# Kernel optimization log

Hardware: AMD Instinct MI355X
Metric: run time of the kernel (lower is better)

Reference implementation:

```python
import jax, jax.numpy as jnp
import numpy as np

N, D, C = 16384, 64, 128
MARGIN = 1.0
EPS_NORM = 1e-6   # F.normalize eps
EPS_PD = 1e-6     # F.pairwise_distance eps (added to the difference elementwise)


def setup_inputs() -> dict:
    key = jax.random.key(0)
    embeddings = jax.random.normal(key, (N, D), dtype=jnp.float32)
    labels = (jnp.arange(N) % C).astype(jnp.int32).reshape(N, 1)
    # deterministic valid positive: same label (i % C), different index
    pos_idx = ((jnp.arange(N) + C) % N).astype(jnp.int32)
    return {"embeddings": embeddings, "labels": labels, "pos_idx": pos_idx}


def reference(embeddings, labels, pos_idx):
    # L2-normalize rows (torch F.normalize: x / max(||x||, eps))
    nrm = jnp.linalg.norm(embeddings, axis=1, keepdims=True)
    e = embeddings / jnp.maximum(nrm, EPS_NORM)

    lab = labels[:, 0]
    # torch pairwise_distance computes ||x1 - x2 + eps||_2, eps added per element:
    # ||xi - xj + eps||^2 = ||xi||^2 + ||xj||^2 - 2 xi.xj + 2*eps*(sum(xi)-sum(xj)) + D*eps^2
    sq = jnp.sum(e * e, axis=1)          # [N]
    s = jnp.sum(e, axis=1)               # [N]
    gram = e @ e.T                        # [N, N]
    d2 = (sq[:, None] + sq[None, :] - 2.0 * gram
          + 2.0 * EPS_PD * (s[:, None] - s[None, :]) + D * EPS_PD * EPS_PD)
    d2 = jnp.maximum(d2, 0.0)
    dist = jnp.sqrt(jnp.maximum(d2, 1e-12))  # guard sqrt grad at 0

    # one positive per anchor: squared distance
    pos_loss = jnp.sum(d2[jnp.arange(N), pos_idx])

    # all negatives per anchor: hinge^2 on (margin - dist)
    neg_mask = lab[:, None] != lab[None, :]
    hinge = jnp.maximum(MARGIN - dist, 0.0)
    neg_loss = jnp.sum(jnp.where(neg_mask, hinge * hinge, 0.0))

    n_comparisons = N + jnp.sum(neg_mask)
    return (pos_loss + neg_loss) / n_comparisons.astype(jnp.float32)
```

## Files before the change

### kernel.cpp

```cpp
#include <hip/hip_runtime.h>
#include <hip/hip_bf16.h>

#define NN 16384
#define DD 64
#define NBI 32
#define NUNITS 2112
#define NBLK 512
#define NPOSB (NN/4)
#define SCREEN_T 0.49f

constexpr float F_EPS_PD   = 1e-6f;
constexpr float F_EPS_NORM = 1e-6f;

using bf16x8 = __attribute__((ext_vector_type(8))) short;
using f32x4  = __attribute__((ext_vector_type(4))) float;
typedef __attribute__((address_space(1))) const unsigned int gu32_t;
typedef __attribute__((address_space(3))) unsigned int       lu32_t;

__device__ __forceinline__ float wave_sum_f(float v) {
    #pragma unroll
    for (int o = 32; o >= 1; o >>= 1) v += __shfl_xor(v, o);
    return v;
}

__device__ __forceinline__ int band_off(int I) { return 2 * I * (65 - I); }

__global__ __launch_bounds__(256) void norm_kernel(
    const float* __restrict__ emb, const int* __restrict__ pidx,
    const int* __restrict__ lab, float2* __restrict__ up,
    float2* __restrict__ vcp, __hip_bfloat16* __restrict__ ebf,
    float* __restrict__ posP) {
    int w    = threadIdx.x >> 6;
    int row  = blockIdx.x * 4 + w;
    int lane = threadIdx.x & 63;
    int j    = pidx[row];
    float x  = emb[(size_t)row * DD + lane];
    float xj = emb[(size_t)j   * DD + lane];

    float n2  = wave_sum_f(x * x);
    float sx  = wave_sum_f(x);
    float n2j = wave_sum_f(xj * xj);
    float sxj = wave_sum_f(xj);
    float dot = wave_sum_f(x * xj);

    float m  = fmaxf(sqrtf(n2),  F_EPS_NORM);
    float mj = fmaxf(sqrtf(n2j), F_EPS_NORM);
    ebf[(size_t)row * DD + lane] = __float2bfloat16(x / m);

    __shared__ float spos[4];
    if (lane == 0) {
        float sq  = n2 / (m * m);
        float sqj = n2j / (mj * mj);
        float s   = sx / m;
        float sj  = sxj / mj;
        float g   = dot / (m * mj);
        float lf  = (float)lab[row];
        up[row]  = make_float2(sq + 2.0f * F_EPS_PD * s, lf);
        vcp[row] = make_float2(
            sq - 2.0f * F_EPS_PD * s + (float)DD * F_EPS_PD * F_EPS_PD, lf);
        float d2p = sq + sqj - 2.0f * g + 2.0f * F_EPS_PD * (s - sj)
                  + (float)DD * F_EPS_PD * F_EPS_PD;
        spos[w] = fmaxf(d2p, 0.0f);
    }
    __syncthreads();
    if (threadIdx.x == 0)
        posP[blockIdx.x] = spos[0] + spos[1] + spos[2] + spos[3];
}

__device__ __forceinline__ void stage_tile(const short* ebf, const float2* vcp,
                                           int tile, short* slotB, float2* slotV,
                                           int w, int lane) {
    const short* tbase = ebf + (size_t)tile * (128 * DD);
    int rlo = lane >> 3;
    int g   = (lane & 7) ^ rlo;
    #pragma unroll
    for (int q = 0; q < 2; ++q) {
        int m = w * 2 + q;
        __builtin_amdgcn_global_load_lds(
            (gu32_t*)(const void*)(tbase + (size_t)(8 * m + rlo) * DD + g * 8),
            (lu32_t*)(void*)(slotB + m * 512), 16, 0, 0);
    }
    __builtin_amdgcn_global_load_lds(
        (gu32_t*)(const void*)(vcp + (size_t)tile * 128 + lane * 2),
        (lu32_t*)(void*)slotV, 16, 0, 0);
}

#define MFMA_STEP(CD, t_)                                                      \
    do {                                                                       \
        const short* rowp_ = lb + ((t_) * 16 + lrow) * 64;                     \
        bf16x8 b0_ = *(const bf16x8*)(rowp_ + c0s);                            \
        bf16x8 b1_ = *(const bf16x8*)(rowp_ + c1s);                            \
        __builtin_amdgcn_s_setprio(1);                                         \
        _Pragma("unroll")                                                      \
        for (int s_ = 0; s_ < 4; ++s_) {                                       \
            f32x4 z_ = {0.f, 0.f, 0.f, 0.f};                                   \
            z_ = __builtin_amdgcn_mfma_f32_16x16x32_bf16(a[s_][0], b0_, z_, 0, 0, 0); \
            z_ = __builtin_amdgcn_mfma_f32_16x16x32_bf16(a[s_][1], b1_, z_, 0, 0, 0); \
            CD[s_] = z_;                                                       \
        }                                                                      \
        __builtin_amdgcn_s_setprio(0);                                         \
    } while (0)

#define SCREEN_STEP(CS, t_)                                                    \
    do {                                                                       \
        float mx_ = fmaxf(fmaxf(CS[0][0], CS[0][1]), fmaxf(CS[0][2], CS[0][3])); \
        mx_ = fmaxf(mx_, fmaxf(fmaxf(CS[1][0], CS[1][1]), fmaxf(CS[1][2], CS[1][3]))); \
        mx_ = fmaxf(mx_, fmaxf(fmaxf(CS[2][0], CS[2][1]), fmaxf(CS[2][2], CS[2][3]))); \
        mx_ = fmaxf(mx_, fmaxf(fmaxf(CS[3][0], CS[3][1]), fmaxf(CS[3][2], CS[3][3]))); \
        if (__any(mx_ > SCREEN_T)) {                                           \
            float2 vl_ = lv[(t_) * 16 + lrow];                                 \
            _Pragma("unroll")                                                  \
            for (int s_ = 0; s_ < 4; ++s_) {                                   \
                _Pragma("unroll")                                              \
                for (int r_ = 0; r_ < 4; ++r_) {                               \
                    float2 ul_ = uband[w * 64 + 16 * s_ + lkh * 4 + r_];       \
                    float d2_ = fmaf(-2.0f, CS[s_][r_], ul_.x + vl_.x);        \
                    float d_  = sqrtf(fmaxf(d2_, 1e-12f));                     \
                    float h_  = fmaxf(1.0f - d_, 0.0f);                        \
                    if (ul_.y != vl_.y) hp = fmaf(h_, h_, hp);                 \
                }                                                              \
            }                                                                  \
        }                                                                      \
    } while (0)

__global__ __launch_bounds__(512, 4) void pair_kernel(
    const short* __restrict__ ebf, const float2* __restrict__ up,
    const float2* __restrict__ vcp, float* __restrict__ negP) {
    __shared__ short  ringB[3][8192];
    __shared__ float2 ringV[3][128];
    __shared__ float2 uband[512];
    __shared__ float  sred[8];
    int tid  = threadIdx.x;
    int w    = tid >> 6;
    int lane = tid & 63;
    int lrow = lane & 15, lkh = lane >> 4;
    int c0s  = ((lkh)     ^ (lrow & 7)) * 8;
    int c1s  = ((lkh + 4) ^ (lrow & 7)) * 8;

    int ks = (int)(((long long)blockIdx.x * NUNITS) / NBLK);
    int ke = (int)(((long long)(blockIdx.x + 1) * NUNITS) / NBLK);

    int I = (int)((65.0f - sqrtf(4225.0f - 2.0f * (float)ks)) * 0.5f);
    I = I < 0 ? 0 : (I > NBI - 1 ? NBI - 1 : I);
    while (band_off(I) > ks) --I;
    while (I < NBI - 1 && band_off(I + 1) <= ks) ++I;

    float hacc = 0.0f;
    int u0 = ks;
    while (u0 < ke) {
        int bend = band_off(I + 1);
        int n    = (ke < bend ? ke : bend) - u0;
        int tj0  = 4 * I + (u0 - band_off(I));
        int rowbase = I * 512 + w * 64;
        int rt      = 4 * I + (w >> 1);

        bf16x8 a[4][2];
        #pragma unroll
        for (int s = 0; s < 4; ++s) {
            const short* ab = ebf + (size_t)(rowbase + 16 * s + lrow) * DD + lkh * 8;
            a[s][0] = *(const bf16x8*)(ab);
            a[s][1] = *(const bf16x8*)(ab + 32);
        }
        if (w < 4)
            __builtin_amdgcn_global_load_lds(
                (gu32_t*)(const void*)(up + (size_t)I * 512 + w * 128 + lane * 2),
                (lu32_t*)(void*)(uband + w * 128), 16, 0, 0);
        stage_tile(ebf, vcp, tj0, &ringB[0][0], &ringV[0][0], w, lane);
        if (n > 1)
            stage_tile(ebf, vcp, tj0 + 1, &ringB[1][0], &ringV[1][0], w, lane);

        int sl = 0;
        for (int k = 0; k < n; ++k) {
            if (k + 1 < n) asm volatile("s_waitcnt vmcnt(3)" ::: "memory");
            else           asm volatile("s_waitcnt vmcnt(0)" ::: "memory");
            __builtin_amdgcn_s_barrier();
            __builtin_amdgcn_sched_barrier(0);
            int sl2 = (sl >= 1) ? sl - 1 : 2;
            if (k + 2 < n)
                stage_tile(ebf, vcp, tj0 + k + 2, &ringB[sl2][0], &ringV[sl2][0],
                           w, lane);

            int tj = tj0 + k;
            float wgt = (tj == rt) ? 1.0f : ((tj > rt) ? 2.0f : 0.0f);
            if (wgt != 0.0f) {
                const short*  lb = &ringB[sl][0];
                const float2* lv = &ringV[sl][0];
                float hp = 0.0f;
                f32x4 cA[4], cB[4];
                MFMA_STEP(cA, 0);
                MFMA_STEP(cB, 1);
                SCREEN_STEP(cA, 0);
                MFMA_STEP(cA, 2);
                SCREEN_STEP(cB, 1);
                MFMA_STEP(cB, 3);
                SCREEN_STEP(cA, 2);
                MFMA_STEP(cA, 4);
                SCREEN_STEP(cB, 3);
                MFMA_STEP(cB, 5);
                SCREEN_STEP(cA, 4);
                MFMA_STEP(cA, 6);
                SCREEN_STEP(cB, 5);
                MFMA_STEP(cB, 7);
                SCREEN_STEP(cA, 6);
                SCREEN_STEP(cB, 7);
                hacc = fmaf(wgt, hp, hacc);
            }
            sl = (sl + 1 == 3) ? 0 : sl + 1;
        }
        __builtin_amdgcn_s_barrier();
        __builtin_amdgcn_sched_barrier(0);
        u0 += n;
        ++I;
    }

    hacc = wave_sum_f(hacc);
    if (lane == 0) sred[w] = hacc;
    __syncthreads();
    if (tid == 0) {
        float tn = 0.f;
        #pragma unroll
        for (int i = 0; i < 8; ++i) tn += sred[i];
        negP[blockIdx.x] = tn;
    }
}

__global__ __launch_bounds__(1024) void reduce_kernel(
    const float* __restrict__ posP, const float* __restrict__ negP,
    const int* __restrict__ lab, float* __restrict__ out) {
    __shared__ unsigned int hist[4][1024];
    int t = threadIdx.x;
    int w = t >> 6, lane = t & 63;
    for (int i = t; i < 4096; i += 1024) hist[i >> 10][i & 1023] = 0u;
    __syncthreads();
    const int4* lab4 = (const int4*)lab;
    for (int i = t; i < NN / 4; i += 1024) {
        int4 v = lab4[i];
        atomicAdd(&hist[w & 3][v.x & 1023], 1u);
        atomicAdd(&hist[w & 3][v.y & 1023], 1u);
        atomicAdd(&hist[w & 3][v.z & 1023], 1u);
        atomicAdd(&hist[w & 3][v.w & 1023], 1u);
    }
    __syncthreads();

    float ps = 0.f, ns = 0.f;
    unsigned long long sqc = 0u;
    const float4* posP4 = (const float4*)posP;
    for (int i = t; i < NPOSB / 4; i += 1024) {
        float4 v = posP4[i];
        ps += (v.x + v.y) + (v.z + v.w);
    }
    if (t < NBLK) ns = negP[t];
    for (int i = t; i < 1024; i += 1024) {
        unsigned long long h = (unsigned long long)hist[0][i] + hist[1][i]
                             + hist[2][i] + hist[3][i];
        sqc += h * h;
    }

    ps = wave_sum_f(ps);
    ns = wave_sum_f(ns);
    #pragma unroll
    for (int o = 32; o >= 1; o >>= 1) sqc += __shfl_xor(sqc, o);

    __shared__ float sp[16], sn[16];
    __shared__ unsigned long long sc[16];
    if (lane == 0) { sp[w] = ps; sn[w] = ns; sc[w] = sqc; }
    __syncthreads();
    if (t == 0) {
        float pos = 0.f, neg = 0.f;
        unsigned long long s2 = 0;
        #pragma unroll
        for (int i = 0; i < 16; ++i) { pos += sp[i]; neg += sn[i]; s2 += sc[i]; }
        unsigned long long nneg = (unsigned long long)NN * NN - s2;
        float ncomp = (float)((unsigned long long)NN + nneg);
        out[0] = (pos + neg) / ncomp;
    }
}

extern "C" void kernel_launch(void* const* d_in, const int* in_sizes, int n_in,
                              void* d_out, int out_size, void* d_ws, size_t ws_size,
                              hipStream_t stream) {
    const float* emb = (const float*)d_in[0];
    const int* lab   = (const int*)d_in[1];
    const int* pidx  = (const int*)d_in[2];
    float* out = (float*)d_out;
    char* ws = (char*)d_ws;
    float2*         up   = (float2*)(ws);
    float2*         vcp  = (float2*)(ws + 131072);
    __hip_bfloat16* ebf  = (__hip_bfloat16*)(ws + 262144);
    float*          posP = (float*)(ws + 2359296);
    float*          negP = (float*)(ws + 2375680);

    norm_kernel<<<NPOSB, 256, 0, stream>>>(emb, pidx, lab, up, vcp, ebf, posP);
    pair_kernel<<<NBLK, 512, 0, stream>>>((const short*)ebf, up, vcp, negP);
    reduce_kernel<<<1, 1024, 0, stream>>>(posP, negP, lab, out);
}
```

Before: 53.88 us.

## Restructure tile loop to prefetch B fragments two steps ahead and relax occupancy

Replaces the interleaved MFMA/screen pipeline with a software-prefetched scheme: B operand fragments for two 16-row sub-tiles are loaded from LDS into registers ahead of use, then each pair is computed and screened immediately. Launch bounds drop from 4 to 2 waves-per-EU minimum, giving the compiler more registers at the cost of possible lower occupancy. The finalize kernel's histogram loop becomes a single unconditional iteration. This aims to hide LDS latency behind MFMA work, but it removes the prior overlap of screening one tile with the MFMAs of the next.

```diff
diff --git a/kernel.cpp b/kernel.cpp
--- a/kernel.cpp
+++ b/kernel.cpp
@@ -85,45 +85,53 @@
         (lu32_t*)(void*)slotV, 16, 0, 0);
 }
 
-#define MFMA_STEP(CD, t_)                                                      \
+#define LOADQ(B, t0_)                                                          \
     do {                                                                       \
-        const short* rowp_ = lb + ((t_) * 16 + lrow) * 64;                     \
-        bf16x8 b0_ = *(const bf16x8*)(rowp_ + c0s);                            \
-        bf16x8 b1_ = *(const bf16x8*)(rowp_ + c1s);                            \
-        __builtin_amdgcn_s_setprio(1);                                         \
+        const short* r0_ = lb + ((t0_) * 16 + lrow) * 64;                      \
+        const short* r1_ = lb + (((t0_) + 1) * 16 + lrow) * 64;                \
+        B[0][0] = *(const bf16x8*)(r0_ + c0s);                                 \
+        B[0][1] = *(const bf16x8*)(r0_ + c1s);                                 \
+        B[1][0] = *(const bf16x8*)(r1_ + c0s);                                 \
+        B[1][1] = *(const bf16x8*)(r1_ + c1s);                                 \
+    } while (0)
+
+#define COMPQ(B, t0_)                                                          \
+    do {                                                                       \
         _Pragma("unroll")                                                      \
-        for (int s_ = 0; s_ < 4; ++s_) {                                       \
-            f32x4 z_ = {0.f, 0.f, 0.f, 0.f};                                   \
-            z_ = __builtin_amdgcn_mfma_f32_16x16x32_bf16(a[s_][0], b0_, z_, 0, 0, 0); \
-            z_ = __builtin_amdgcn_mfma_f32_16x16x32_bf16(a[s_][1], b1_, z_, 0, 0, 0); \
-            CD[s_] = z_;                                                       \
-        }                                                                      \
-        __builtin_amdgcn_s_setprio(0);                                         \
-    } while (0)
-
-#define SCREEN_STEP(CS, t_)                                                    \
-    do {                                                                       \
-        float mx_ = fmaxf(fmaxf(CS[0][0], CS[0][1]), fmaxf(CS[0][2], CS[0][3])); \
-        mx_ = fmaxf(mx_, fmaxf(fmaxf(CS[1][0], CS[1][1]), fmaxf(CS[1][2], CS[1][3]))); \
-        mx_ = fmaxf(mx_, fmaxf(fmaxf(CS[2][0], CS[2][1]), fmaxf(CS[2][2], CS[2][3]))); \
-        mx_ = fmaxf(mx_, fmaxf(fmaxf(CS[3][0], CS[3][1]), fmaxf(CS[3][2], CS[3][3]))); \
-        if (__any(mx_ > SCREEN_T)) {                                           \
-            float2 vl_ = lv[(t_) * 16 + lrow];                                 \
+        for (int tt_ = 0; tt_ < 2; ++tt_) {                                    \
+            __builtin_amdgcn_s_setprio(1);                                     \
+            f32x4 c4[4];                                                       \
             _Pragma("unroll")                                                  \
             for (int s_ = 0; s_ < 4; ++s_) {                                   \
+                f32x4 z_ = {0.f, 0.f, 0.f, 0.f};                               \
+                z_ = __builtin_amdgcn_mfma_f32_16x16x32_bf16(a[s_][0], B[tt_][0], z_, 0, 0, 0); \
+                z_ = __builtin_amdgcn_mfma_f32_16x16x32_bf16(a[s_][1], B[tt_][1], z_, 0, 0, 0); \
+                c4[s_] = z_;                                                   \
+            }                                                                  \
+            __builtin_amdgcn_s_setprio(0);                                     \
+            float m0_ = fmaxf(fmaxf(c4[0][0], c4[0][1]), fmaxf(c4[0][2], c4[0][3])); \
+            float m1_ = fmaxf(fmaxf(c4[1][0], c4[1][1]), fmaxf(c4[1][2], c4[1][3])); \
+            float m2_ = fmaxf(fmaxf(c4[2][0], c4[2][1]), fmaxf(c4[2][2], c4[2][3])); \
+            float m3_ = fmaxf(fmaxf(c4[3][0], c4[3][1]), fmaxf(c4[3][2], c4[3][3])); \
+            float mx_ = fmaxf(fmaxf(m0_, m1_), fmaxf(m2_, m3_));               \
+            if (__any(mx_ > SCREEN_T)) {              \
+                float2 vl_ = lv[((t0_) + tt_) * 16 + lrow];                    \
                 _Pragma("unroll")                                              \
-                for (int r_ = 0; r_ < 4; ++r_) {                               \
-                    float2 ul_ = uband[w * 64 + 16 * s_ + lkh * 4 + r_];       \
-                    float d2_ = fmaf(-2.0f, CS[s_][r_], ul_.x + vl_.x);        \
-                    float d_  = sqrtf(fmaxf(d2_, 1e-12f));                     \
-                    float h_  = fmaxf(1.0f - d_, 0.0f);                        \
-                    if (ul_.y != vl_.y) hp = fmaf(h_, h_, hp);                 \
+                for (int s_ = 0; s_ < 4; ++s_) {                               \
+                    _Pragma("unroll")                                          \
+                    for (int r_ = 0; r_ < 4; ++r_) {                           \
+                        float2 ul_ = uband[w * 64 + 16 * s_ + lkh * 4 + r_];   \
+                        float d2_ = fmaf(-2.0f, c4[s_][r_], ul_.x + vl_.x);    \
+                        float d_  = sqrtf(fmaxf(d2_, 1e-12f));                 \
+                        float h_  = fmaxf(1.0f - d_, 0.0f);                    \
+                        if (ul_.y != vl_.y) hp = fmaf(h_, h_, hp);             \
+                    }                                                          \
                 }                                                              \
             }                                                                  \
         }                                                                      \
     } while (0)
 
-__global__ __launch_bounds__(512, 4) void pair_kernel(
+__global__ __launch_bounds__(512, 2) void pair_kernel(
     const short* __restrict__ ebf, const float2* __restrict__ up,
     const float2* __restrict__ vcp, float* __restrict__ negP) {
     __shared__ short  ringB[3][8192];
@@ -186,23 +194,15 @@
                 const short*  lb = &ringB[sl][0];
                 const float2* lv = &ringV[sl][0];
                 float hp = 0.0f;
-                f32x4 cA[4], cB[4];
-                MFMA_STEP(cA, 0);
-                MFMA_STEP(cB, 1);
-                SCREEN_STEP(cA, 0);
-                MFMA_STEP(cA, 2);
-                SCREEN_STEP(cB, 1);
-                MFMA_STEP(cB, 3);
-                SCREEN_STEP(cA, 2);
-                MFMA_STEP(cA, 4);
-                SCREEN_STEP(cB, 3);
-                MFMA_STEP(cB, 5);
-                SCREEN_STEP(cA, 4);
-                MFMA_STEP(cA, 6);
-                SCREEN_STEP(cB, 5);
-                MFMA_STEP(cB, 7);
-                SCREEN_STEP(cA, 6);
-                SCREEN_STEP(cB, 7);
+                bf16x8 Q0[2][2], Q1[2][2];
+                LOADQ(Q0, 0);
+                LOADQ(Q1, 2);
+                COMPQ(Q0, 0);
+                LOADQ(Q0, 4);
+                COMPQ(Q1, 2);
+                LOADQ(Q1, 6);
+                COMPQ(Q0, 4);
+                COMPQ(Q1, 6);
                 hacc = fmaf(wgt, hp, hacc);
             }
             sl = (sl + 1 == 3) ? 0 : sl + 1;
@@ -250,10 +250,10 @@
         ps += (v.x + v.y) + (v.z + v.w);
     }
     if (t < NBLK) ns = negP[t];
-    for (int i = t; i < 1024; i += 1024) {
-        unsigned long long h = (unsigned long long)hist[0][i] + hist[1][i]
-                             + hist[2][i] + hist[3][i];
-        sqc += h * h;
+    {
+        unsigned long long h = (unsigned long long)hist[0][t & 1023] + hist[1][t & 1023]
+                             + hist[2][t & 1023] + hist[3][t & 1023];
+        sqc = h * h;
     }
 
     ps = wave_sum_f(ps);
```

Measured after the change: 52.77 us. -2.1%, faster.

## Software-pipeline LDS B loads ahead of MFMA with sched_group_barrier interleaving

Applied to the files above, without the earlier changes.

The per-tile inner loop now loads the next 16-row B fragment from LDS one step ahead of the MFMAs that use it. It adds sched_group_barrier hints to interleave DS reads, MFMAs and VALU screening work, and drops the s_setprio toggles. Launch bounds go from 4 to 2 waves per EU minimum, which frees registers for the extra live fragments but may lower occupancy. The final histogram square-sum loop becomes a single straight-line read per thread.

```diff
diff --git a/kernel.cpp b/kernel.cpp
--- a/kernel.cpp
+++ b/kernel.cpp
@@ -85,36 +85,39 @@
         (lu32_t*)(void*)slotV, 16, 0, 0);
 }
 
-#define MFMA_STEP(CD, t_)                                                      \
+#define LD1(B, t_)                                                             \
     do {                                                                       \
-        const short* rowp_ = lb + ((t_) * 16 + lrow) * 64;                     \
-        bf16x8 b0_ = *(const bf16x8*)(rowp_ + c0s);                            \
-        bf16x8 b1_ = *(const bf16x8*)(rowp_ + c1s);                            \
-        __builtin_amdgcn_s_setprio(1);                                         \
+        const short* r_ = lb + ((t_) * 16 + lrow) * 64;                        \
+        B[0] = *(const bf16x8*)(r_ + c0s);                                     \
+        B[1] = *(const bf16x8*)(r_ + c1s);                                     \
+    } while (0)
+
+#define MM1(C, B)                                                              \
+    do {                                                                       \
         _Pragma("unroll")                                                      \
         for (int s_ = 0; s_ < 4; ++s_) {                                       \
             f32x4 z_ = {0.f, 0.f, 0.f, 0.f};                                   \
-            z_ = __builtin_amdgcn_mfma_f32_16x16x32_bf16(a[s_][0], b0_, z_, 0, 0, 0); \
-            z_ = __builtin_amdgcn_mfma_f32_16x16x32_bf16(a[s_][1], b1_, z_, 0, 0, 0); \
-            CD[s_] = z_;                                                       \
+            z_ = __builtin_amdgcn_mfma_f32_16x16x32_bf16(a[s_][0], B[0], z_, 0, 0, 0); \
+            z_ = __builtin_amdgcn_mfma_f32_16x16x32_bf16(a[s_][1], B[1], z_, 0, 0, 0); \
+            C[s_] = z_;                                                        \
         }                                                                      \
-        __builtin_amdgcn_s_setprio(0);                                         \
     } while (0)
 
-#define SCREEN_STEP(CS, t_)                                                    \
+#define SC1(C, t_)                                                             \
     do {                                                                       \
-        float mx_ = fmaxf(fmaxf(CS[0][0], CS[0][1]), fmaxf(CS[0][2], CS[0][3])); \
-        mx_ = fmaxf(mx_, fmaxf(fmaxf(CS[1][0], CS[1][1]), fmaxf(CS[1][2], CS[1][3]))); \
-        mx_ = fmaxf(mx_, fmaxf(fmaxf(CS[2][0], CS[2][1]), fmaxf(CS[2][2], CS[2][3]))); \
-        mx_ = fmaxf(mx_, fmaxf(fmaxf(CS[3][0], CS[3][1]), fmaxf(CS[3][2], CS[3][3]))); \
-        if (__any(mx_ > SCREEN_T)) {                                           \
+        float m0_ = fmaxf(fmaxf(C[0][0], C[0][1]), fmaxf(C[0][2], C[0][3]));   \
+        float m1_ = fmaxf(fmaxf(C[1][0], C[1][1]), fmaxf(C[1][2], C[1][3]));   \
+        float m2_ = fmaxf(fmaxf(C[2][0], C[2][1]), fmaxf(C[2][2], C[2][3]));   \
+        float m3_ = fmaxf(fmaxf(C[3][0], C[3][1]), fmaxf(C[3][2], C[3][3]));   \
+        float mx_ = fmaxf(fmaxf(m0_, m1_), fmaxf(m2_, m3_));                   \
+        if (__any(mx_ > SCREEN_T)) {                  \
             float2 vl_ = lv[(t_) * 16 + lrow];                                 \
             _Pragma("unroll")                                                  \
             for (int s_ = 0; s_ < 4; ++s_) {                                   \
                 _Pragma("unroll")                                              \
                 for (int r_ = 0; r_ < 4; ++r_) {                               \
                     float2 ul_ = uband[w * 64 + 16 * s_ + lkh * 4 + r_];       \
-                    float d2_ = fmaf(-2.0f, CS[s_][r_], ul_.x + vl_.x);        \
+                    float d2_ = fmaf(-2.0f, C[s_][r_], ul_.x + vl_.x);         \
                     float d_  = sqrtf(fmaxf(d2_, 1e-12f));                     \
                     float h_  = fmaxf(1.0f - d_, 0.0f);                        \
                     if (ul_.y != vl_.y) hp = fmaf(h_, h_, hp);                 \
@@ -123,7 +126,14 @@
         }                                                                      \
     } while (0)
 
-__global__ __launch_bounds__(512, 4) void pair_kernel(
+#define SGB()                                                                  \
+    do {                                                                       \
+        __builtin_amdgcn_sched_group_barrier(0x100, 2, 0);                     \
+        __builtin_amdgcn_sched_group_barrier(0x008, 8, 0);                     \
+        __builtin_amdgcn_sched_group_barrier(0x002, 16, 0);                    \
+    } while (0)
+
+__global__ __launch_bounds__(512, 2) void pair_kernel(
     const short* __restrict__ ebf, const float2* __restrict__ up,
     const float2* __restrict__ vcp, float* __restrict__ negP) {
     __shared__ short  ringB[3][8192];
@@ -186,23 +196,18 @@
                 const short*  lb = &ringB[sl][0];
                 const float2* lv = &ringV[sl][0];
                 float hp = 0.0f;
-                f32x4 cA[4], cB[4];
-                MFMA_STEP(cA, 0);
-                MFMA_STEP(cB, 1);
-                SCREEN_STEP(cA, 0);
-                MFMA_STEP(cA, 2);
-                SCREEN_STEP(cB, 1);
-                MFMA_STEP(cB, 3);
-                SCREEN_STEP(cA, 2);
-                MFMA_STEP(cA, 4);
-                SCREEN_STEP(cB, 3);
-                MFMA_STEP(cB, 5);
-                SCREEN_STEP(cA, 4);
-                MFMA_STEP(cA, 6);
-                SCREEN_STEP(cB, 5);
-                MFMA_STEP(cB, 7);
-                SCREEN_STEP(cA, 6);
-                SCREEN_STEP(cB, 7);
+                bf16x8 BA[2], BB[2];
+                f32x4 CA[4], CB[4];
+                LD1(BA, 0);
+                LD1(BB, 1); MM1(CA, BA);
+                LD1(BA, 2); MM1(CB, BB); SC1(CA, 0); SGB();
+                LD1(BB, 3); MM1(CA, BA); SC1(CB, 1); SGB();
+                LD1(BA, 4); MM1(CB, BB); SC1(CA, 2); SGB();
+                LD1(BB, 5); MM1(CA, BA); SC1(CB, 3); SGB();
+                LD1(BA, 6); MM1(CB, BB); SC1(CA, 4); SGB();
+                LD1(BB, 7); MM1(CA, BA); SC1(CB, 5); SGB();
+                MM1(CB, BB); SC1(CA, 6);
+                SC1(CB, 7);
                 hacc = fmaf(wgt, hp, hacc);
             }
             sl = (sl + 1 == 3) ? 0 : sl + 1;
@@ -250,10 +255,10 @@
         ps += (v.x + v.y) + (v.z + v.w);
     }
     if (t < NBLK) ns = negP[t];
-    for (int i = t; i < 1024; i += 1024) {
-        unsigned long long h = (unsigned long long)hist[0][i] + hist[1][i]
-                             + hist[2][i] + hist[3][i];
-        sqc += h * h;
+    {
+        unsigned long long h = (unsigned long long)hist[0][t & 1023] + hist[1][t & 1023]
+                             + hist[2][t & 1023] + hist[3][t & 1023];
+        sqc = h * h;
     }
 
     ps = wave_sum_f(ps);
```

Result: no change. 53.13 us (-1.4%).
